# Optimization experiments

Measured on AMD Instinct MI355X. Metric: run time of the kernel, lower is better.

Reference implementation:

```python
import jax, jax.numpy as jnp
import numpy as np

NC = 80
NA = 3
BOX_GAIN, CLS_GAIN, OBJ_GAIN = 7.5, 0.5, 1.0
GAMMA = 1.5
LS = 0.0
EPS = 1e-7
ANCHORS = np.array([[[10, 13], [16, 30], [33, 23]],
                    [[30, 61], [62, 45], [59, 119]],
                    [[116, 90], [156, 198], [373, 326]]], dtype=np.float32)


def bce_logits(x, t):
    # numerically stable BCE-with-logits, elementwise
    return jnp.maximum(x, 0.0) - x * t + jnp.log1p(jnp.exp(-jnp.abs(x)))


def iou_cxcywh(b1, b2, eps=EPS):
    b1x1, b1x2 = b1[..., 0] - b1[..., 2] / 2, b1[..., 0] + b1[..., 2] / 2
    b1y1, b1y2 = b1[..., 1] - b1[..., 3] / 2, b1[..., 1] + b1[..., 3] / 2
    b2x1, b2x2 = b2[..., 0] - b2[..., 2] / 2, b2[..., 0] + b2[..., 2] / 2
    b2y1, b2y2 = b2[..., 1] - b2[..., 3] / 2, b2[..., 1] + b2[..., 3] / 2
    inter = jnp.clip(jnp.minimum(b1x2, b2x2) - jnp.maximum(b1x1, b2x1), 0.0) * \
            jnp.clip(jnp.minimum(b1y2, b2y2) - jnp.maximum(b1y1, b2y1), 0.0)
    w1, h1 = b1x2 - b1x1, b1y2 - b1y1 + eps
    w2, h2 = b2x2 - b2x1, b2y2 - b2y1 + eps
    union = w1 * h1 + w2 * h2 - inter + eps
    return inter / union


def _scale_loss(pred, targets, anchors):
    B, C, h, w = pred.shape
    p = pred.reshape(B, NA, NC + 5, h, w).transpose(0, 1, 3, 4, 2)  # [B,3,h,w,nc+5]
    pobj = p[..., 4]

    N = targets.shape[0]
    scale = jnp.array([w, h, w, h], dtype=pred.dtype)
    g = targets[:, 2:6] * scale  # grid-space cx,cy,w,h
    gx, gy = g[:, 0], g[:, 1]
    valid = (gx >= 0) & (gx < w) & (gy >= 0) & (gy < h)
    gi = jnp.clip(jnp.floor(gx).astype(jnp.int32), 0, w - 1)
    gj = jnp.clip(jnp.floor(gy).astype(jnp.int32), 0, h - 1)
    bidx = jnp.clip(targets[:, 0].astype(jnp.int32), 0, B - 1)
    cls = jnp.clip(targets[:, 1].astype(jnp.int32), 0, NC - 1)

    # each GT is assigned to all 3 anchors -> M = 3N rows
    rep = lambda v: jnp.repeat(v, NA, axis=0)
    bM, giM, gjM, clsM, maskM = rep(bidx), rep(gi), rep(gj), rep(cls), rep(valid)
    aiM = jnp.tile(jnp.arange(NA), N)
    anchM = anchors[aiM]                             # [M,2]
    txyM = rep(g[:, :2] - jnp.floor(g[:, :2]))       # cell-relative offsets
    twhM = rep(g[:, 2:4])
    mf = maskM.astype(pred.dtype)
    n_valid = mf.sum()

    # objectness target grid (duplicates collapse to 1 via max, like repeated set)
    tobj = jnp.zeros((B, NA, h, w), pred.dtype).at[bM, aiM, gjM, giM].max(mf)
    loss_obj = bce_logits(pobj, tobj).mean() * OBJ_GAIN

    ps = p[bM, aiM, gjM, giM]                        # [M, nc+5]
    ps_box, ps_cls = ps[:, :4], ps[:, 5:]

    # focal classification loss
    t = jax.nn.one_hot(clsM, NC, dtype=pred.dtype)
    if LS > 0:
        t = t * (1 - LS) + LS / NC
    ce = bce_logits(ps_cls, t)
    focal = (1.0 - jnp.exp(-ce)) ** GAMMA * ce       # [M, nc]
    row_sum = (focal * mf[:, None]).sum(-1)          # [M]
    loss_cls = jnp.where(n_valid > 0,
                         row_sum.sum() / (jnp.maximum(n_valid, 1.0) * NC),
                         0.0) * CLS_GAIN

    # per-class focal means (rows grouped by GT class)
    seg_ids = jnp.where(maskM, clsM, NC)
    seg_sum = jax.ops.segment_sum(row_sum, seg_ids, num_segments=NC + 1)[:NC]
    seg_cnt = jax.ops.segment_sum(mf, seg_ids, num_segments=NC + 1)[:NC]
    per_class = jnp.where(seg_cnt > 0,
                          seg_sum / (jnp.maximum(seg_cnt, 1.0) * NC),
                          0.0) * CLS_GAIN

    # box (IoU) loss
    pxy = jax.nn.sigmoid(ps_box[:, :2]) * 2.0 - 0.5
    pwh = (jax.nn.sigmoid(ps_box[:, 2:4]) * 2.0) ** 2 * anchM
    pbox = jnp.concatenate([pxy, pwh], axis=-1)
    tbox = jnp.concatenate([txyM, twhM], axis=-1)
    iou = iou_cxcywh(pbox, tbox)
    loss_box = jnp.where(n_valid > 0,
                         ((1.0 - iou) * mf).sum() / jnp.maximum(n_valid, 1.0),
                         0.0) * BOX_GAIN

    return loss_box, loss_cls, loss_obj, per_class


def setup_inputs() -> dict:
    key = jax.random.key(0)
    k0, k1, k2, kb, kc, kxy, kwh = jax.random.split(key, 7)
    B, N = 16, 800
    p0 = jax.random.normal(k0, (B, NA * (NC + 5), 80, 80), jnp.float32)
    p1 = jax.random.normal(k1, (B, NA * (NC + 5), 40, 40), jnp.float32)
    p2 = jax.random.normal(k2, (B, NA * (NC + 5), 20, 20), jnp.float32)
    bcol = jax.random.randint(kb, (N, 1), 0, B).astype(jnp.float32)
    ccol = jax.random.randint(kc, (N, 1), 0, NC).astype(jnp.float32)
    xy = jax.random.uniform(kxy, (N, 2), jnp.float32, 0.02, 0.98)
    wh = jax.random.uniform(kwh, (N, 2), jnp.float32, 0.02, 0.30)
    targets = jnp.concatenate([bcol, ccol, xy, wh], axis=1)  # [N,6]
    return {"p0": p0, "p1": p1, "p2": p2, "targets": targets}


def reference(p0, p1, p2, targets):
    anchors = jnp.asarray(ANCHORS)
    lb = lc = lo = 0.0
    pc = jnp.zeros((NC,), jnp.float32)
    for i, pred in enumerate((p0, p1, p2)):
        b, c, o, per_class = _scale_loss(pred, targets, anchors[i])
        lb, lc, lo = lb + b, lc + c, lo + o
        pc = pc + per_class
    total = lb + lc + lo
    # [loss, loss_box, loss_cls, loss_obj, per-class cls losses...]
    return jnp.concatenate([jnp.stack([total, lb, lc, lo]), pc])
```

## Files before the change

### kernel.cpp

```cpp
#include <hip/hip_runtime.h>
#include <math.h>

#define NC 80
#define TCOLS 6
#define RPB 15

__device__ __constant__ float c_anch[3][3][2] = {
  {{10.f,13.f},{16.f,30.f},{33.f,23.f}},
  {{30.f,61.f},{62.f,45.f},{59.f,119.f}},
  {{116.f,90.f},{156.f,198.f},{373.f,326.f}}
};

#define SEGOFF  0
#define SLOTOFF 512

__device__ __forceinline__ float fbce0(float x) {
  return fmaxf(x, 0.f) + __logf(1.f + __expf(-fabsf(x)));
}
__device__ __forceinline__ float fbce(float x, float t) {
  return fmaxf(x, 0.f) - x * t + __logf(1.f + __expf(-fabsf(x)));
}
__device__ __forceinline__ float ffocal(float x, float t) {
  float ce = fbce(x, t);
  float u  = 1.f - __expf(-ce);
  return u * __builtin_amdgcn_sqrtf(u) * ce;
}

__global__ void k_init(float* __restrict__ ws) {
  for (int k = threadIdx.x; k < 6*NC; k += 256) ws[SEGOFF + k] = 0.f;
}

__global__ __launch_bounds__(1024, 8)
void k_fused(const float* __restrict__ p0, const float* __restrict__ p1,
             const float* __restrict__ p2, const float* __restrict__ tgt,
             int N, int B, int RB, float* __restrict__ ws) {
  const int bid = blockIdx.x;
  const int tid = threadIdx.x;
  float* slot = ws + SLOTOFF + bid * 16;
  float* seg  = ws + SEGOFF;

  if (bid < RB) {
    __shared__ float l_box[3], l_cls[3], l_nv[3], s_obj;
    if (tid < 3) { l_box[tid]=0.f; l_cls[tid]=0.f; l_nv[tid]=0.f; }
    __syncthreads();
    int wv   = tid >> 6;
    int lane = tid & 63;
    if (wv < RPB) {
      int row   = bid * RPB + wv;
      int nrows = 9 * N;
      if (row < nrows) {
        int rps = N * 3;
        int s   = row / rps;
        int rem = row - s * rps;
        int n   = rem / 3;
        int a   = rem - n * 3;
        int w   = (s == 0) ? 80 : ((s == 1) ? 40 : 20);
        int hw  = w * w;
        const float* pred = (s == 0) ? p0 : ((s == 1) ? p1 : p2);
        float fw = (float)w;
        float gx = tgt[n*TCOLS + 2] * fw, gy = tgt[n*TCOLS + 3] * fw;
        if (gx >= 0.f && gx < fw && gy >= 0.f && gy < fw) {
          float gw = tgt[n*TCOLS + 4] * fw, gh = tgt[n*TCOLS + 5] * fw;
          int gi  = min(max((int)floorf(gx), 0), w - 1);
          int gj  = min(max((int)floorf(gy), 0), w - 1);
          int b   = min(max((int)tgt[n*TCOLS + 0], 0), B - 1);
          int cls = min(max((int)tgt[n*TCOLS + 1], 0), NC - 1);
          size_t base = (size_t)(b*255 + a*85) * hw + (size_t)(gj*w + gi);

          float x0  = pred[base + (size_t)(5 + lane) * hw];
          float x1  = (lane < 16) ? pred[base + (size_t)(69 + lane) * hw] : 0.f;
          float bxv = (lane < 4)  ? pred[base + (size_t)lane * hw] : 0.f;

          float rs = ffocal(x0, (lane == cls) ? 1.f : 0.f);
          if (lane < 16) rs += ffocal(x1, ((64 + lane) == cls) ? 1.f : 0.f);
          for (int off = 32; off > 0; off >>= 1) rs += __shfl_xor(rs, off, 64);

          float bx = __shfl(bxv, 0, 64), by = __shfl(bxv, 1, 64);
          float bw = __shfl(bxv, 2, 64), bh = __shfl(bxv, 3, 64);
          if (lane == 0) {
            float sx = 1.f/(1.f + __expf(-bx));
            float sy = 1.f/(1.f + __expf(-by));
            float sw = 1.f/(1.f + __expf(-bw));
            float sh = 1.f/(1.f + __expf(-bh));
            float px = sx*2.f - 0.5f, py = sy*2.f - 0.5f;
            float aw = c_anch[s][a][0], ah = c_anch[s][a][1];
            float pw = (sw*2.f)*(sw*2.f)*aw, ph = (sh*2.f)*(sh*2.f)*ah;
            float txf = gx - floorf(gx), tyf = gy - floorf(gy);
            float b1x1 = px - pw*0.5f, b1x2 = px + pw*0.5f;
            float b1y1 = py - ph*0.5f, b1y2 = py + ph*0.5f;
            float b2x1 = txf - gw*0.5f, b2x2 = txf + gw*0.5f;
            float b2y1 = tyf - gh*0.5f, b2y2 = tyf + gh*0.5f;
            float iw = fmaxf(fminf(b1x2, b2x2) - fmaxf(b1x1, b2x1), 0.f);
            float ih = fmaxf(fminf(b1y2, b2y2) - fmaxf(b1y1, b2y1), 0.f);
            float inter = iw * ih;
            float w1 = b1x2 - b1x1, h1 = b1y2 - b1y1 + 1e-7f;
            float w2 = b2x2 - b2x1, h2 = b2y2 - b2y1 + 1e-7f;
            float uni = w1*h1 + w2*h2 - inter + 1e-7f;
            float iou = inter / uni;

            atomicAdd(&l_box[s], 1.f - iou);
            atomicAdd(&l_cls[s], rs);
            atomicAdd(&l_nv[s],  1.f);
            atomicAdd(&seg[       s*NC + cls], rs);
            atomicAdd(&seg[3*NC + s*NC + cls], 1.f);
          }
        }
      }
    } else {
      const int n0 = B*3*6400, n1 = B*3*1600, n2 = B*3*400;
      const int total4 = (n0 + n1 + n2) >> 2;
      const int opb = (total4 + RB - 1) / RB;
      const float i0 = 1.f/(float)n0, i1 = 1.f/(float)n1, i2 = 1.f/(float)n2;
      int start = bid * opb;
      int end   = min(start + opb, total4);
      float local = 0.f;
      for (int i = start + lane; i < end; i += 64) {
        int e = i << 2;
        const float* pred; int idx, hw; float inv;
        if (e < n0)         { pred = p0; idx = e;           hw = 6400; inv = i0; }
        else if (e < n0+n1) { pred = p1; idx = e - n0;      hw = 1600; inv = i1; }
        else                { pred = p2; idx = e - n0 - n1; hw = 400;  inv = i2; }
        int ba = idx / hw, pix = idx - ba * hw;
        int b = ba / 3, a = ba - b * 3;
        const float4 x4 = *(const float4*)&pred[(size_t)(b*255 + a*85 + 4) * hw + pix];
        local += (fbce0(x4.x) + fbce0(x4.y) + fbce0(x4.z) + fbce0(x4.w)) * inv;
      }
      for (int off = 32; off > 0; off >>= 1) local += __shfl_xor(local, off, 64);
      if (lane == 0) s_obj = local;
    }
    __syncthreads();
    if (tid < 3) {
      slot[tid    ] = l_box[tid];
      slot[tid + 3] = l_cls[tid];
      slot[tid + 6] = l_nv[tid];
    }
    if (tid == 0) { slot[9] = s_obj; slot[10] = 0.f; }
  } else {
    const int bimg = bid - RB;
    __shared__ unsigned cmask[264];
    __shared__ float red[16];
    for (int k = tid; k < 264; k += 1024) cmask[k] = 0u;
    __syncthreads();
    float corr = 0.f;
    for (int n = tid; n < N; n += 1024) {
      int b = min(max((int)tgt[n*TCOLS + 0], 0), B - 1);
      if (b != bimg) continue;
      float tx = tgt[n*TCOLS + 2], ty = tgt[n*TCOLS + 3];
      #pragma unroll
      for (int s = 0; s < 3; ++s) {
        int w  = (s == 0) ? 80 : ((s == 1) ? 40 : 20);
        int hw = w * w;
        float fw = (float)w;
        float gx = tx * fw, gy = ty * fw;
        if (!(gx >= 0.f && gx < fw && gy >= 0.f && gy < fw)) continue;
        int gi = min(max((int)floorf(gx), 0), w - 1);
        int gj = min(max((int)floorf(gy), 0), w - 1);
        int cell = gj * w + gi;
        int bit  = ((s == 0) ? 0 : ((s == 1) ? 6400 : 8000)) + cell;
        unsigned m = 1u << (bit & 31);
        unsigned old = atomicOr(&cmask[bit >> 5], m);
        if (!(old & m)) {
          const float* pred = (s == 0) ? p0 : ((s == 1) ? p1 : p2);
          float inv = 1.f / (float)(B * 3 * hw);
          float sum = pred[(size_t)(bimg*255 +   4) * hw + cell]
                    + pred[(size_t)(bimg*255 +  89) * hw + cell]
                    + pred[(size_t)(bimg*255 + 174) * hw + cell];
          corr -= sum * inv;
        }
      }
    }
    for (int off = 32; off > 0; off >>= 1) corr += __shfl_xor(corr, off, 64);
    if ((tid & 63) == 0) red[tid >> 6] = corr;
    __syncthreads();
    if (tid < 10) slot[tid] = 0.f;
    if (tid == 0) {
      float t = 0.f;
      for (int k = 0; k < 16; ++k) t += red[k];
      slot[10] = t;
    }
  }
}

__global__ __launch_bounds__(512)
void k_final(const float* __restrict__ ws, int nblk, float* __restrict__ out) {
  __shared__ float red[8][11];
  __shared__ float sS[11];
  const int tid  = threadIdx.x;
  const int lane = tid & 63;
  const int wv   = tid >> 6;

  float v[11];
  #pragma unroll
  for (int j = 0; j < 11; ++j) v[j] = 0.f;
  for (int b = tid; b < nblk; b += 512) {
    const float* slot = ws + SLOTOFF + b * 16;
    #pragma unroll
    for (int j = 0; j < 11; ++j) v[j] += slot[j];
  }
  #pragma unroll
  for (int j = 0; j < 11; ++j)
    for (int off = 32; off > 0; off >>= 1) v[j] += __shfl_xor(v[j], off, 64);
  if (lane == 0)
    #pragma unroll
    for (int j = 0; j < 11; ++j) red[wv][j] = v[j];
  __syncthreads();
  if (tid < 11) {
    float t = 0.f;
    for (int k = 0; k < 8; ++k) t += red[k][tid];
    sS[tid] = t;
  }
  __syncthreads();

  if (tid == 0) {
    float lo = sS[9] + sS[10];
    float lb = 0.f, lc = 0.f;
    for (int s = 0; s < 3; ++s) {
      float nv  = sS[6 + s];
      float nvm = fmaxf(nv, 1.f);
      if (nv > 0.f) {
        lb += sS[s]     / nvm * 7.5f;
        lc += sS[3 + s] / (nvm * (float)NC) * 0.5f;
      }
    }
    out[0] = lb + lc + lo;
    out[1] = lb;
    out[2] = lc;
    out[3] = lo;
  }
  if (tid < NC) {
    float pc = 0.f;
    for (int s = 0; s < 3; ++s) {
      float cnt = ws[SEGOFF + 3*NC + s*NC + tid];
      if (cnt > 0.f)
        pc += ws[SEGOFF + s*NC + tid] / (fmaxf(cnt, 1.f) * (float)NC) * 0.5f;
    }
    out[4 + tid] = pc;
  }
}

extern "C" void kernel_launch(void* const* d_in, const int* in_sizes, int n_in,
                              void* d_out, int out_size, void* d_ws, size_t ws_size,
                              hipStream_t stream) {
  const float* p0  = (const float*)d_in[0];
  const float* p1  = (const float*)d_in[1];
  const float* p2  = (const float*)d_in[2];
  const float* tgt = (const float*)d_in[3];
  int N = in_sizes[3] / TCOLS;
  int B = in_sizes[0] / (255 * 6400);
  float* out = (float*)d_out;
  float* ws  = (float*)d_ws;

  int nrows = 9 * N;
  int RB   = (nrows + RPB - 1) / RPB;
  int grid = RB + B;

  k_init <<<1, 256, 0, stream>>>(ws);
  k_fused<<<grid, 1024, 0, stream>>>(p0, p1, p2, tgt, N, B, RB, ws);
  k_final<<<1, 512, 0, stream>>>(ws, grid, out);
}
```

Measured before the change: 36.57 us.

## Replace global segment atomics with per-row records and dedicate objectness blocks

Each assignment row now writes its class key and focal-loss sum to a per-row record instead of doing atomicAdd into a zeroed global per-class table. The single k_final block then reduces those records with shared-memory atomics, which removes the k_init launch and the global atomics. The objectness BCE sweep moves off the spare wave of every row block into 16 dedicated blocks, with the correction blocks hardcoded at 16. The trade-offs are that the tail kernel does a serial pass over 9N records, the objectness sweep runs on fewer blocks, and CORRB assumes B equals 16.

```diff
diff --git a/kernel.cpp b/kernel.cpp
--- a/kernel.cpp
+++ b/kernel.cpp
@@ -4,6 +4,11 @@
 #define NC 80
 #define TCOLS 6
 #define RPB 15
+#define CORRB 16
+#define OBJB 16
+
+#define SLOTOFF 0
+#define RECOFF  8192
 
 __device__ __constant__ float c_anch[3][3][2] = {
   {{10.f,13.f},{16.f,30.f},{33.f,23.f}},
@@ -11,9 +16,6 @@
   {{116.f,90.f},{156.f,198.f},{373.f,326.f}}
 };
 
-#define SEGOFF  0
-#define SLOTOFF 512
-
 __device__ __forceinline__ float fbce0(float x) {
   return fmaxf(x, 0.f) + __logf(1.f + __expf(-fabsf(x)));
 }
@@ -24,10 +26,6 @@
   float ce = fbce(x, t);
   float u  = 1.f - __expf(-ce);
   return u * __builtin_amdgcn_sqrtf(u) * ce;
-}
-
-__global__ void k_init(float* __restrict__ ws) {
-  for (int k = threadIdx.x; k < 6*NC; k += 256) ws[SEGOFF + k] = 0.f;
 }
 
 __global__ __launch_bounds__(1024, 8)
@@ -37,96 +35,79 @@
   const int bid = blockIdx.x;
   const int tid = threadIdx.x;
   float* slot = ws + SLOTOFF + bid * 16;
-  float* seg  = ws + SEGOFF;
+  __shared__ float red[16];
 
   if (bid < RB) {
-    __shared__ float l_box[3], l_cls[3], l_nv[3], s_obj;
+    __shared__ float l_box[3], l_cls[3], l_nv[3];
     if (tid < 3) { l_box[tid]=0.f; l_cls[tid]=0.f; l_nv[tid]=0.f; }
     __syncthreads();
-    int wv   = tid >> 6;
-    int lane = tid & 63;
-    if (wv < RPB) {
-      int row   = bid * RPB + wv;
-      int nrows = 9 * N;
-      if (row < nrows) {
-        int rps = N * 3;
-        int s   = row / rps;
-        int rem = row - s * rps;
-        int n   = rem / 3;
-        int a   = rem - n * 3;
-        int w   = (s == 0) ? 80 : ((s == 1) ? 40 : 20);
-        int hw  = w * w;
-        const float* pred = (s == 0) ? p0 : ((s == 1) ? p1 : p2);
-        float fw = (float)w;
-        float gx = tgt[n*TCOLS + 2] * fw, gy = tgt[n*TCOLS + 3] * fw;
-        if (gx >= 0.f && gx < fw && gy >= 0.f && gy < fw) {
-          float gw = tgt[n*TCOLS + 4] * fw, gh = tgt[n*TCOLS + 5] * fw;
-          int gi  = min(max((int)floorf(gx), 0), w - 1);
-          int gj  = min(max((int)floorf(gy), 0), w - 1);
-          int b   = min(max((int)tgt[n*TCOLS + 0], 0), B - 1);
-          int cls = min(max((int)tgt[n*TCOLS + 1], 0), NC - 1);
-          size_t base = (size_t)(b*255 + a*85) * hw + (size_t)(gj*w + gi);
-
-          float x0  = pred[base + (size_t)(5 + lane) * hw];
-          float x1  = (lane < 16) ? pred[base + (size_t)(69 + lane) * hw] : 0.f;
-          float bxv = (lane < 4)  ? pred[base + (size_t)lane * hw] : 0.f;
-
-          float rs = ffocal(x0, (lane == cls) ? 1.f : 0.f);
-          if (lane < 16) rs += ffocal(x1, ((64 + lane) == cls) ? 1.f : 0.f);
-          for (int off = 32; off > 0; off >>= 1) rs += __shfl_xor(rs, off, 64);
-
-          float bx = __shfl(bxv, 0, 64), by = __shfl(bxv, 1, 64);
-          float bw = __shfl(bxv, 2, 64), bh = __shfl(bxv, 3, 64);
-          if (lane == 0) {
-            float sx = 1.f/(1.f + __expf(-bx));
-            float sy = 1.f/(1.f + __expf(-by));
-            float sw = 1.f/(1.f + __expf(-bw));
-            float sh = 1.f/(1.f + __expf(-bh));
-            float px = sx*2.f - 0.5f, py = sy*2.f - 0.5f;
-            float aw = c_anch[s][a][0], ah = c_anch[s][a][1];
-            float pw = (sw*2.f)*(sw*2.f)*aw, ph = (sh*2.f)*(sh*2.f)*ah;
-            float txf = gx - floorf(gx), tyf = gy - floorf(gy);
-            float b1x1 = px - pw*0.5f, b1x2 = px + pw*0.5f;
-            float b1y1 = py - ph*0.5f, b1y2 = py + ph*0.5f;
-            float b2x1 = txf - gw*0.5f, b2x2 = txf + gw*0.5f;
-            float b2y1 = tyf - gh*0.5f, b2y2 = tyf + gh*0.5f;
-            float iw = fmaxf(fminf(b1x2, b2x2) - fmaxf(b1x1, b2x1), 0.f);
-            float ih = fmaxf(fminf(b1y2, b2y2) - fmaxf(b1y1, b2y1), 0.f);
-            float inter = iw * ih;
-            float w1 = b1x2 - b1x1, h1 = b1y2 - b1y1 + 1e-7f;
-            float w2 = b2x2 - b2x1, h2 = b2y2 - b2y1 + 1e-7f;
-            float uni = w1*h1 + w2*h2 - inter + 1e-7f;
-            float iou = inter / uni;
-
-            atomicAdd(&l_box[s], 1.f - iou);
-            atomicAdd(&l_cls[s], rs);
-            atomicAdd(&l_nv[s],  1.f);
-            atomicAdd(&seg[       s*NC + cls], rs);
-            atomicAdd(&seg[3*NC + s*NC + cls], 1.f);
-          }
+    int wv    = tid >> 6;
+    int lane  = tid & 63;
+    int row   = bid * RPB + wv;
+    int nrows = 9 * N;
+    float keyout = -1.f, rsout = 0.f;
+    if (wv < RPB && row < nrows) {
+      int rps = N * 3;
+      int s   = row / rps;
+      int rem = row - s * rps;
+      int n   = rem / 3;
+      int a   = rem - n * 3;
+      int w   = (s == 0) ? 80 : ((s == 1) ? 40 : 20);
+      int hw  = w * w;
+      const float* pred = (s == 0) ? p0 : ((s == 1) ? p1 : p2);
+      float fw = (float)w;
+      float gx = tgt[n*TCOLS + 2] * fw, gy = tgt[n*TCOLS + 3] * fw;
+      if (gx >= 0.f && gx < fw && gy >= 0.f && gy < fw) {
+        float gw = tgt[n*TCOLS + 4] * fw, gh = tgt[n*TCOLS + 5] * fw;
+        int gi  = min(max((int)floorf(gx), 0), w - 1);
+        int gj  = min(max((int)floorf(gy), 0), w - 1);
+        int b   = min(max((int)tgt[n*TCOLS + 0], 0), B - 1);
+        int cls = min(max((int)tgt[n*TCOLS + 1], 0), NC - 1);
+        size_t base = (size_t)(b*255 + a*85) * hw + (size_t)(gj*w + gi);
+
+        float x0  = pred[base + (size_t)(5 + lane) * hw];
+        float x1  = (lane < 16) ? pred[base + (size_t)(69 + lane) * hw] : 0.f;
+        float bxv = (lane < 4)  ? pred[base + (size_t)lane * hw] : 0.f;
+
+        float rs = ffocal(x0, (lane == cls) ? 1.f : 0.f);
+        if (lane < 16) rs += ffocal(x1, ((64 + lane) == cls) ? 1.f : 0.f);
+        for (int off = 32; off > 0; off >>= 1) rs += __shfl_xor(rs, off, 64);
+
+        keyout = (float)(s * NC + cls);
+        rsout  = rs;
+
+        float bx = __shfl(bxv, 0, 64), by = __shfl(bxv, 1, 64);
+        float bw = __shfl(bxv, 2, 64), bh = __shfl(bxv, 3, 64);
+        if (lane == 0) {
+          float sx = 1.f/(1.f + __expf(-bx));
+          float sy = 1.f/(1.f + __expf(-by));
+          float sw = 1.f/(1.f + __expf(-bw));
+          float sh = 1.f/(1.f + __expf(-bh));
+          float px = sx*2.f - 0.5f, py = sy*2.f - 0.5f;
+          float aw = c_anch[s][a][0], ah = c_anch[s][a][1];
+          float pw = (sw*2.f)*(sw*2.f)*aw, ph = (sh*2.f)*(sh*2.f)*ah;
+          float txf = gx - floorf(gx), tyf = gy - floorf(gy);
+          float b1x1 = px - pw*0.5f, b1x2 = px + pw*0.5f;
+          float b1y1 = py - ph*0.5f, b1y2 = py + ph*0.5f;
+          float b2x1 = txf - gw*0.5f, b2x2 = txf + gw*0.5f;
+          float b2y1 = tyf - gh*0.5f, b2y2 = tyf + gh*0.5f;
+          float iw = fmaxf(fminf(b1x2, b2x2) - fmaxf(b1x1, b2x1), 0.f);
+          float ih = fmaxf(fminf(b1y2, b2y2) - fmaxf(b1y1, b2y1), 0.f);
+          float inter = iw * ih;
+          float w1 = b1x2 - b1x1, h1 = b1y2 - b1y1 + 1e-7f;
+          float w2 = b2x2 - b2x1, h2 = b2y2 - b2y1 + 1e-7f;
+          float uni = w1*h1 + w2*h2 - inter + 1e-7f;
+          float iou = inter / uni;
+
+          atomicAdd(&l_box[s], 1.f - iou);
+          atomicAdd(&l_cls[s], rs);
+          atomicAdd(&l_nv[s],  1.f);
         }
       }
-    } else {
-      const int n0 = B*3*6400, n1 = B*3*1600, n2 = B*3*400;
-      const int total4 = (n0 + n1 + n2) >> 2;
-      const int opb = (total4 + RB - 1) / RB;
-      const float i0 = 1.f/(float)n0, i1 = 1.f/(float)n1, i2 = 1.f/(float)n2;
-      int start = bid * opb;
-      int end   = min(start + opb, total4);
-      float local = 0.f;
-      for (int i = start + lane; i < end; i += 64) {
-        int e = i << 2;
-        const float* pred; int idx, hw; float inv;
-        if (e < n0)         { pred = p0; idx = e;           hw = 6400; inv = i0; }
-        else if (e < n0+n1) { pred = p1; idx = e - n0;      hw = 1600; inv = i1; }
-        else                { pred = p2; idx = e - n0 - n1; hw = 400;  inv = i2; }
-        int ba = idx / hw, pix = idx - ba * hw;
-        int b = ba / 3, a = ba - b * 3;
-        const float4 x4 = *(const float4*)&pred[(size_t)(b*255 + a*85 + 4) * hw + pix];
-        local += (fbce0(x4.x) + fbce0(x4.y) + fbce0(x4.z) + fbce0(x4.w)) * inv;
-      }
-      for (int off = 32; off > 0; off >>= 1) local += __shfl_xor(local, off, 64);
-      if (lane == 0) s_obj = local;
+    }
+    if (wv < RPB && row < nrows && lane == 0) {
+      ws[RECOFF + row*2    ] = keyout;
+      ws[RECOFF + row*2 + 1] = rsout;
     }
     __syncthreads();
     if (tid < 3) {
@@ -134,11 +115,10 @@
       slot[tid + 3] = l_cls[tid];
       slot[tid + 6] = l_nv[tid];
     }
-    if (tid == 0) { slot[9] = s_obj; slot[10] = 0.f; }
-  } else {
+    if (tid == 0) { slot[9] = 0.f; slot[10] = 0.f; }
+  } else if (bid < RB + CORRB) {
     const int bimg = bid - RB;
     __shared__ unsigned cmask[264];
-    __shared__ float red[16];
     for (int k = tid; k < 264; k += 1024) cmask[k] = 0u;
     __syncthreads();
     float corr = 0.f;
@@ -178,16 +158,47 @@
       for (int k = 0; k < 16; ++k) t += red[k];
       slot[10] = t;
     }
+  } else {
+    const int ob = bid - RB - CORRB;
+    const int n0 = B*3*6400, n1 = B*3*1600, n2 = B*3*400;
+    const int total4 = (n0 + n1 + n2) >> 2;
+    const float i0 = 1.f/(float)n0, i1 = 1.f/(float)n1, i2 = 1.f/(float)n2;
+    float local = 0.f;
+    for (int i = ob * 1024 + tid; i < total4; i += OBJB * 1024) {
+      int e = i << 2;
+      const float* pred; int idx, hw; float inv;
+      if (e < n0)         { pred = p0; idx = e;           hw = 6400; inv = i0; }
+      else if (e < n0+n1) { pred = p1; idx = e - n0;      hw = 1600; inv = i1; }
+      else                { pred = p2; idx = e - n0 - n1; hw = 400;  inv = i2; }
+      int ba = idx / hw, pix = idx - ba * hw;
+      int b = ba / 3, a = ba - b * 3;
+      const float4 x4 = *(const float4*)&pred[(size_t)(b*255 + a*85 + 4) * hw + pix];
+      local += (fbce0(x4.x) + fbce0(x4.y) + fbce0(x4.z) + fbce0(x4.w)) * inv;
+    }
+    for (int off = 32; off > 0; off >>= 1) local += __shfl_xor(local, off, 64);
+    if ((tid & 63) == 0) red[tid >> 6] = local;
+    __syncthreads();
+    if (tid < 10) slot[tid] = 0.f;
+    if (tid == 10) slot[10] = 0.f;
+    if (tid == 0) {
+      float t = 0.f;
+      for (int k = 0; k < 16; ++k) t += red[k];
+      slot[9] = t;
+    }
   }
 }
 
 __global__ __launch_bounds__(512)
-void k_final(const float* __restrict__ ws, int nblk, float* __restrict__ out) {
+void k_final(const float* __restrict__ ws, int nblk, int nrows,
+             float* __restrict__ out) {
+  __shared__ float seg_sum[3*NC], seg_cnt[3*NC];
   __shared__ float red[8][11];
   __shared__ float sS[11];
   const int tid  = threadIdx.x;
   const int lane = tid & 63;
   const int wv   = tid >> 6;
+
+  for (int k = tid; k < 3*NC; k += 512) { seg_sum[k] = 0.f; seg_cnt[k] = 0.f; }
 
   float v[11];
   #pragma unroll
@@ -203,6 +214,16 @@
   if (lane == 0)
     #pragma unroll
     for (int j = 0; j < 11; ++j) red[wv][j] = v[j];
+  __syncthreads();
+
+  for (int r = tid; r < nrows; r += 512) {
+    float key = ws[RECOFF + r*2];
+    if (key >= 0.f) {
+      int k = (int)key;
+      atomicAdd(&seg_sum[k], ws[RECOFF + r*2 + 1]);
+      atomicAdd(&seg_cnt[k], 1.f);
+    }
+  }
   __syncthreads();
   if (tid < 11) {
     float t = 0.f;
@@ -230,9 +251,9 @@
   if (tid < NC) {
     float pc = 0.f;
     for (int s = 0; s < 3; ++s) {
-      float cnt = ws[SEGOFF + 3*NC + s*NC + tid];
+      float cnt = seg_cnt[s*NC + tid];
       if (cnt > 0.f)
-        pc += ws[SEGOFF + s*NC + tid] / (fmaxf(cnt, 1.f) * (float)NC) * 0.5f;
+        pc += seg_sum[s*NC + tid] / (fmaxf(cnt, 1.f) * (float)NC) * 0.5f;
     }
     out[4 + tid] = pc;
   }
@@ -252,9 +273,8 @@
 
   int nrows = 9 * N;
   int RB   = (nrows + RPB - 1) / RPB;
-  int grid = RB + B;
-
-  k_init <<<1, 256, 0, stream>>>(ws);
+  int grid = RB + CORRB + OBJB;
+
   k_fused<<<grid, 1024, 0, stream>>>(p0, p1, p2, tgt, N, B, RB, ws);
-  k_final<<<1, 512, 0, stream>>>(ws, grid, out);
-}
+  k_final<<<1, 512, 0, stream>>>(ws, grid, nrows, out);
+}
```

Result: slower. 46.24 us (+26.4%).
